# Kernel optimization log

Hardware: AMD Instinct MI355X
Metric: run time of the kernel (lower is better)

The kernel has to match this reference:

```python
import jax, jax.numpy as jnp
import numpy as np
from jax.scipy.special import logsumexp

DEN_SCALE = 1.0  # den_scale from LFMMILoss.__init__


def _log_marginal(em, seqlens, logA, log_start, log_final):
    """Forward (alpha) recursion of a WFSA in log space.
    em: [B,T,S] per-state emission log-likelihoods; logA: [S,S] or [B,S,S].
    Returns per-sequence log-marginal [B].
    """
    B, T, S = em.shape
    alpha0 = log_start + em[:, 0]  # [B,S]

    def step(alpha, xs):
        em_t, t = xs
        # [B,S,1] + [.,S,S] -> logsumexp over source state
        new = logsumexp(alpha[:, :, None] + logA, axis=1) + em_t
        alpha = jnp.where((t < seqlens)[:, None], new, alpha)
        return alpha, None

    em_t_first = jnp.swapaxes(em, 0, 1)  # [T,B,S]
    alpha, _ = jax.lax.scan(step, alpha0, (em_t_first[1:], jnp.arange(1, T)))
    return logsumexp(alpha + log_final, axis=1)  # [B]


def _fsm_logprob(x, seqlens, logA, log_start, log_final, pdf_ids):
    B, T, _ = x.shape
    if pdf_ids.ndim == 1:  # shared graph (denominator)
        em = x[:, :, pdf_ids]  # [B,T,S]
    else:  # per-utterance graphs (numerators), pdf_ids: [B,S]
        S = pdf_ids.shape[-1]
        idx = jnp.broadcast_to(pdf_ids[:, None, :], (B, T, S))
        em = jnp.take_along_axis(x, idx, axis=2)
    return _log_marginal(em, seqlens, logA, log_start, log_final)


def setup_inputs() -> dict:
    key = jax.random.key(0)
    ks = jax.random.split(key, 10)
    B, T, C = 16, 500, 2048
    S_num, S_den = 64, 512
    inp = jax.random.normal(ks[0], (B, T, C), jnp.float32)
    seqlengths = jax.random.randint(ks[1], (B,), T // 2, T + 1, jnp.int32)
    num_logA = jax.nn.log_softmax(jax.random.normal(ks[2], (B, S_num, S_num), jnp.float32), axis=-1)
    num_log_start = jax.nn.log_softmax(jax.random.normal(ks[3], (B, S_num), jnp.float32), axis=-1)
    num_log_final = jax.nn.log_softmax(jax.random.normal(ks[4], (B, S_num), jnp.float32), axis=-1)
    num_pdf_ids = jax.random.randint(ks[5], (B, S_num), 0, C, jnp.int32)
    den_logA = jax.nn.log_softmax(jax.random.normal(ks[6], (S_den, S_den), jnp.float32), axis=-1)
    den_log_start = jax.nn.log_softmax(jax.random.normal(ks[7], (S_den,), jnp.float32), axis=-1)
    den_log_final = jax.nn.log_softmax(jax.random.normal(ks[8], (S_den,), jnp.float32), axis=-1)
    den_pdf_ids = jax.random.randint(ks[9], (S_den,), 0, C, jnp.int32)
    return {
        "input": inp, "seqlengths": seqlengths,
        "num_logA": num_logA, "num_log_start": num_log_start,
        "num_log_final": num_log_final, "num_pdf_ids": num_pdf_ids,
        "den_logA": den_logA, "den_log_start": den_log_start,
        "den_log_final": den_log_final, "den_pdf_ids": den_pdf_ids,
    }


def reference(input, seqlengths, num_logA, num_log_start, num_log_final,
              num_pdf_ids, den_logA, den_log_start, den_log_final, den_pdf_ids):
    x = jnp.clip(input, -30.0, 30.0)
    num_llh = _fsm_logprob(x, seqlengths, num_logA, num_log_start, num_log_final, num_pdf_ids).sum()
    den_llh = _fsm_logprob(x, seqlengths, den_logA, den_log_start, den_log_final, den_pdf_ids).sum()
    return -(num_llh - DEN_SCALE * den_llh)
```

## Files before the change

kernel.cpp:

```cpp
#include <hip/hip_runtime.h>
#include <math.h>

#define BB 16
#define TT 500
#define CC 2048
#define SN 64
#define SD 512
#define NGRP 16
#define NCB 8
#define NDEN 128
#define NTHR 512
#define SHIFTC 30.0f

#define WSF_DACC   32768
#define WSF_DSCALE 32784
#define WSF_NACC   32800
#define WSF_NSCALE 32816

#define AL(p) __hip_atomic_load((p), __ATOMIC_RELAXED, __HIP_MEMORY_SCOPE_AGENT)
#define AS(p, v) __hip_atomic_store((p), (v), __ATOMIC_RELAXED, __HIP_MEMORY_SCOPE_AGENT)

__device__ __forceinline__ float wave_max(float v) {
  #pragma unroll
  for (int off = 32; off > 0; off >>= 1) v = fmaxf(v, __shfl_xor(v, off, 64));
  return v;
}
__device__ __forceinline__ float wave_sum(float v) {
  #pragma unroll
  for (int off = 32; off > 0; off >>= 1) v += __shfl_xor(v, off, 64);
  return v;
}
__device__ __forceinline__ unsigned long long pk(unsigned tag, float v) {
  return ((unsigned long long)tag << 32) | (unsigned long long)__float_as_uint(v);
}
__device__ __forceinline__ float clamp30(float v) {
  return fminf(fmaxf(v, -30.f), 30.f);
}

__global__ __launch_bounds__(NTHR, 1) void fsm_fwd(
    const float* __restrict__ x, const int* __restrict__ seqlens,
    const float* __restrict__ nA, const float* __restrict__ nls,
    const float* __restrict__ nlf, const int* __restrict__ npdf,
    const float* __restrict__ dA, const float* __restrict__ dls,
    const float* __restrict__ dlf, const int* __restrict__ dpdf,
    unsigned long long* __restrict__ p64, float* __restrict__ wsf)
{
  __shared__ float prt[2][8 * 64];
  __shared__ float pmx[2][8];
  const int tid = threadIdx.x;
  const int lane = tid & 63, wv = tid >> 6;

  if (blockIdx.x < NDEN) {
    const int g  = blockIdx.x & 15;
    const int cb = blockIdx.x >> 4;
    const int j0 = cb * 64;

    float Areg[64];
    {
      const float* Ap = dA + (wv * 64) * SD + j0 + lane;
      #pragma unroll
      for (int k = 0; k < 64; ++k)
        Areg[k] = __expf(Ap[k * SD]);
    }

    unsigned long long* gb0 = p64 + (size_t)g * SD;
    unsigned long long* gb1 = p64 + (size_t)(NGRP + g) * SD;

    int pdfj = 0, sl = 0; float lfj = 0.f, pcur = 0.f, scale = SHIFTC;
    if (wv == 0) {
      pdfj = dpdf[j0 + lane];
      lfj  = dlf[j0 + lane];
      sl   = seqlens[g];
      float xv = clamp30(x[g * (TT * CC) + pdfj]);
      pcur = __expf(dls[j0 + lane] + xv - SHIFTC);
      AS(gb0 + j0 + lane, pk(0u, pcur));
    }

    for (int t = 1; t < TT; ++t) {
      unsigned long long* gin  = (t & 1) ? gb0 : gb1;
      unsigned long long* gout = (t & 1) ? gb1 : gb0;
      float xv = 0.f;
      if (wv == 0)
        xv = clamp30(x[g * (TT * CC) + t * CC + pdfj]);

      const unsigned tg = (unsigned)(t - 1);
      unsigned long long* pa = gin + wv * 64 + lane;
      unsigned long long w;
      for (;;) {
        w = AL(pa);
        if ((unsigned)(w >> 32) == tg) break;
        __builtin_amdgcn_s_sleep(1);
      }
      float pv = __uint_as_float((unsigned)w);

      float cm = wave_max(pv);
      if (lane == 0) pmx[t & 1][wv] = cm;

      float q = 0.f;
      #pragma unroll
      for (int k = 0; k < 64; ++k) {
        float pk_ = __uint_as_float(__builtin_amdgcn_readlane(__float_as_uint(pv), k));
        q = fmaf(pk_, Areg[k], q);
      }
      prt[t & 1][wv * 64 + lane] = q;
      __syncthreads();

      if (wv == 0) {
        const float* pb = prt[t & 1];
        float qq = 0.f;
        #pragma unroll
        for (int w8 = 0; w8 < 8; ++w8) qq += pb[w8 * 64 + lane];
        float m = pmx[t & 1][0];
        #pragma unroll
        for (int w8 = 1; w8 < 8; ++w8) m = fmaxf(m, pmx[t & 1][w8]);
        float lm = __logf(m);
        if (t < sl) {
          pcur = qq * __expf(xv - SHIFTC - lm);
          scale += SHIFTC + lm;
        }
        AS(gout + j0 + lane, pk((unsigned)t, pcur));
      }
    }
    if (wv == 0) {
      float part = wave_sum(pcur * __expf(lfj));
      if (lane == 0) {
        atomicAdd(wsf + WSF_DACC + g, part);
        if (cb == 0) wsf[WSF_DSCALE + g] = scale;
      }
    }
  } else {
    const int b = blockIdx.x - NDEN;
    if (wv != 0) return;

    float Areg[64];
    {
      const float* Ap = nA + b * SN * SN + lane;
      #pragma unroll
      for (int i = 0; i < 64; ++i)
        Areg[i] = __expf(Ap[i * SN]);
    }
    const int   pdfj = npdf[b * SN + lane];
    const float lfj  = nlf[b * SN + lane];
    const int   sl   = seqlens[b];
    float xv = clamp30(x[b * (TT * CC) + pdfj]);
    float pcur = __expf(nls[b * SN + lane] + xv - SHIFTC);
    float scale = SHIFTC;

    for (int t = 1; t < TT; ++t) {
      xv = clamp30(x[b * (TT * CC) + t * CC + pdfj]);
      float pold = pcur;
      float q = 0.f;
      #pragma unroll
      for (int i = 0; i < 64; ++i) {
        float pi = __uint_as_float(__builtin_amdgcn_readlane(__float_as_uint(pold), i));
        q = fmaf(pi, Areg[i], q);
      }
      float lm = __logf(wave_max(pold));
      if (t < sl) {
        pcur = q * __expf(xv - SHIFTC - lm);
        scale += SHIFTC + lm;
      }
    }
    float part = wave_sum(pcur * __expf(lfj));
    if (lane == 0) {
      wsf[WSF_NACC + b]   = part;
      wsf[WSF_NSCALE + b] = scale;
    }
  }
}

__global__ void fsm_final(const float* __restrict__ wsf, float* __restrict__ out) {
  const int tid = threadIdx.x;
  float v = 0.f;
  if (tid < 16)
    v = -(wsf[WSF_NSCALE + tid] + __logf(wsf[WSF_NACC + tid]));
  else if (tid < 32)
    v = (wsf[WSF_DSCALE + tid - 16] + __logf(wsf[WSF_DACC + tid - 16]));
  v = wave_sum(v);
  if (tid == 0) out[0] = v;
}

extern "C" void kernel_launch(void* const* d_in, const int* in_sizes, int n_in,
                              void* d_out, int out_size, void* d_ws, size_t ws_size,
                              hipStream_t stream) {
  const float* x    = (const float*)d_in[0];
  const int*   sql  = (const int*)d_in[1];
  const float* nA   = (const float*)d_in[2];
  const float* nls  = (const float*)d_in[3];
  const float* nlf  = (const float*)d_in[4];
  const int*   npdf = (const int*)d_in[5];
  const float* dA   = (const float*)d_in[6];
  const float* dls  = (const float*)d_in[7];
  const float* dlf  = (const float*)d_in[8];
  const int*   dpdf = (const int*)d_in[9];
  float* out = (float*)d_out;
  unsigned long long* p64 = (unsigned long long*)d_ws;
  float* wsf = (float*)d_ws;
  (void)in_sizes; (void)n_in; (void)out_size; (void)ws_size;

  hipMemsetAsync((char*)d_ws + 131072, 0, 256, stream);
  fsm_fwd<<<NDEN + BB, NTHR, 0, stream>>>(x, sql, nA, nls, nlf, npdf,
                                          dA, dls, dlf, dpdf, p64, wsf);
  fsm_final<<<1, 64, 0, stream>>>(wsf, out);
}
```

Baseline: 892.4 us.

## Replace gather-then-reduce alpha exchange with distributed partial-sum reduce-scatter across blocks

The denominator recursion no longer funnels each step through wave 0. Previously wave 0 published 64 alpha values, every wave polled the full vector from global memory, and partials were reduced in LDS. Now every wave keeps its own 64-state slice of alpha and publishes per-(block, wave) partial products tagged with the step. Each wave then polls and sums the eight partials for its slice, so the serial wave-0 stage and one LDS reduction round are removed from the critical per-step path. In exchange there is more global polling traffic (eight tagged loads per lane), a larger workspace, and redundant alpha state in all eight blocks per group. Because each group's final sum is written by a single block, the atomic accumulation and the workspace memset are dropped.

```diff
diff --git a/kernel.cpp b/kernel.cpp
--- a/kernel.cpp
+++ b/kernel.cpp
@@ -6,16 +6,15 @@
 #define CC 2048
 #define SN 64
 #define SD 512
-#define NGRP 16
-#define NCB 8
 #define NDEN 128
 #define NTHR 512
 #define SHIFTC 30.0f
 
-#define WSF_DACC   32768
-#define WSF_DSCALE 32784
-#define WSF_NACC   32800
-#define WSF_NSCALE 32816
+#define PBUFO ((size_t)(16 * 8 * 8 * 64))
+#define WSF_DACC   262144
+#define WSF_DSCALE 262160
+#define WSF_NACC   262176
+#define WSF_NSCALE 262192
 
 #define AL(p) __hip_atomic_load((p), __ATOMIC_RELAXED, __HIP_MEMORY_SCOPE_AGENT)
 #define AS(p, v) __hip_atomic_store((p), (v), __ATOMIC_RELAXED, __HIP_MEMORY_SCOPE_AGENT)
@@ -45,8 +44,8 @@
     const float* __restrict__ dlf, const int* __restrict__ dpdf,
     unsigned long long* __restrict__ p64, float* __restrict__ wsf)
 {
-  __shared__ float prt[2][8 * 64];
   __shared__ float pmx[2][8];
+  __shared__ float red[8];
   const int tid = threadIdx.x;
   const int lane = tid & 63, wv = tid >> 6;
 
@@ -54,79 +53,92 @@
     const int g  = blockIdx.x & 15;
     const int cb = blockIdx.x >> 4;
     const int j0 = cb * 64;
+    const int i0 = wv * 64;
+    const int si = i0 + lane;
 
     float Areg[64];
     {
-      const float* Ap = dA + (wv * 64) * SD + j0 + lane;
+      const float* Ap = dA + (size_t)i0 * SD + j0 + lane;
       #pragma unroll
       for (int k = 0; k < 64; ++k)
-        Areg[k] = __expf(Ap[k * SD]);
-    }
-
-    unsigned long long* gb0 = p64 + (size_t)g * SD;
-    unsigned long long* gb1 = p64 + (size_t)(NGRP + g) * SD;
-
-    int pdfj = 0, sl = 0; float lfj = 0.f, pcur = 0.f, scale = SHIFTC;
-    if (wv == 0) {
-      pdfj = dpdf[j0 + lane];
-      lfj  = dlf[j0 + lane];
-      sl   = seqlens[g];
-      float xv = clamp30(x[g * (TT * CC) + pdfj]);
-      pcur = __expf(dls[j0 + lane] + xv - SHIFTC);
-      AS(gb0 + j0 + lane, pk(0u, pcur));
-    }
+        Areg[k] = __expf(Ap[(size_t)k * SD]);
+    }
+
+    const int   pdfj = dpdf[si];
+    const float lfj  = dlf[si];
+    const int   sl   = seqlens[g];
+    const float* xb  = x + (size_t)g * TT * CC;
+
+    float pwin  = __expf(dls[si] + clamp30(xb[pdfj]) - SHIFTC);
+    float scale = SHIFTC;
+    {
+      float wm = wave_max(pwin);
+      if (lane == 0) pmx[0][wv] = wm;
+    }
+    __syncthreads();
+    float lm;
+    {
+      float m = pmx[0][0];
+      #pragma unroll
+      for (int r = 1; r < 8; ++r) m = fmaxf(m, pmx[0][r]);
+      lm = __logf(m);
+    }
+
+    unsigned long long* myrow = p64 + (((size_t)g * 8 + cb) * 8 + wv) * 64;
+    unsigned long long* prows = p64 + (((size_t)g * 8 + wv) * 8) * 64;
 
     for (int t = 1; t < TT; ++t) {
-      unsigned long long* gin  = (t & 1) ? gb0 : gb1;
-      unsigned long long* gout = (t & 1) ? gb1 : gb0;
-      float xv = 0.f;
-      if (wv == 0)
-        xv = clamp30(x[g * (TT * CC) + t * CC + pdfj]);
-
-      const unsigned tg = (unsigned)(t - 1);
-      unsigned long long* pa = gin + wv * 64 + lane;
-      unsigned long long w;
-      for (;;) {
-        w = AL(pa);
-        if ((unsigned)(w >> 32) == tg) break;
-        __builtin_amdgcn_s_sleep(1);
-      }
-      float pv = __uint_as_float((unsigned)w);
-
-      float cm = wave_max(pv);
-      if (lane == 0) pmx[t & 1][wv] = cm;
+      const size_t bo = (t & 1) ? PBUFO : 0;
+      float xq = clamp30(xb[(size_t)t * CC + pdfj]);
 
       float q = 0.f;
       #pragma unroll
       for (int k = 0; k < 64; ++k) {
-        float pk_ = __uint_as_float(__builtin_amdgcn_readlane(__float_as_uint(pv), k));
-        q = fmaf(pk_, Areg[k], q);
-      }
-      prt[t & 1][wv * 64 + lane] = q;
+        float pv = __uint_as_float(__builtin_amdgcn_readlane(__float_as_uint(pwin), k));
+        q = fmaf(pv, Areg[k], q);
+      }
+      AS(myrow + bo + lane, pk((unsigned)t, q));
+
+      unsigned long long wr[8];
+      const unsigned tg = (unsigned)t;
+      unsigned long long* pr = prows + bo + lane;
+      unsigned miss = 0xFFu;
+      do {
+        #pragma unroll
+        for (int r = 0; r < 8; ++r)
+          if (miss & (1u << r)) wr[r] = AL(pr + r * 64);
+        #pragma unroll
+        for (int r = 0; r < 8; ++r)
+          if ((miss & (1u << r)) && (unsigned)(wr[r] >> 32) == tg) miss &= ~(1u << r);
+      } while (miss);
+
+      float s = 0.f;
+      #pragma unroll
+      for (int r = 0; r < 8; ++r) s += __uint_as_float((unsigned)wr[r]);
+      if (t < sl) {
+        pwin = s * __expf(xq - SHIFTC - lm);
+        scale += SHIFTC + lm;
+      }
+      float wm = wave_max(pwin);
+      if (lane == 0) pmx[t & 1][wv] = wm;
       __syncthreads();
-
-      if (wv == 0) {
-        const float* pb = prt[t & 1];
-        float qq = 0.f;
-        #pragma unroll
-        for (int w8 = 0; w8 < 8; ++w8) qq += pb[w8 * 64 + lane];
+      {
         float m = pmx[t & 1][0];
         #pragma unroll
-        for (int w8 = 1; w8 < 8; ++w8) m = fmaxf(m, pmx[t & 1][w8]);
-        float lm = __logf(m);
-        if (t < sl) {
-          pcur = qq * __expf(xv - SHIFTC - lm);
-          scale += SHIFTC + lm;
-        }
-        AS(gout + j0 + lane, pk((unsigned)t, pcur));
-      }
-    }
-    if (wv == 0) {
-      float part = wave_sum(pcur * __expf(lfj));
-      if (lane == 0) {
-        atomicAdd(wsf + WSF_DACC + g, part);
-        if (cb == 0) wsf[WSF_DSCALE + g] = scale;
-      }
+        for (int r = 1; r < 8; ++r) m = fmaxf(m, pmx[t & 1][r]);
+        lm = __logf(m);
+      }
+    }
+
+    float part = wave_sum(pwin * __expf(lfj));
+    if (lane == 0) red[wv] = part;
+    __syncthreads();
+    if (cb == 0 && tid == 0) {
+      float sum = 0.f;
+      #pragma unroll
+      for (int r = 0; r < 8; ++r) sum += red[r];
+      wsf[WSF_DACC + g]   = sum;
+      wsf[WSF_DSCALE + g] = scale;
     }
   } else {
     const int b = blockIdx.x - NDEN;
@@ -142,12 +154,12 @@
     const int   pdfj = npdf[b * SN + lane];
     const float lfj  = nlf[b * SN + lane];
     const int   sl   = seqlens[b];
-    float xv = clamp30(x[b * (TT * CC) + pdfj]);
+    float xv = clamp30(x[(size_t)b * TT * CC + pdfj]);
     float pcur = __expf(nls[b * SN + lane] + xv - SHIFTC);
     float scale = SHIFTC;
 
     for (int t = 1; t < TT; ++t) {
-      xv = clamp30(x[b * (TT * CC) + t * CC + pdfj]);
+      xv = clamp30(x[(size_t)b * TT * CC + t * CC + pdfj]);
       float pold = pcur;
       float q = 0.f;
       #pragma unroll
@@ -198,7 +210,6 @@
   float* wsf = (float*)d_ws;
   (void)in_sizes; (void)n_in; (void)out_size; (void)ws_size;
 
-  hipMemsetAsync((char*)d_ws + 131072, 0, 256, stream);
   fsm_fwd<<<NDEN + BB, NTHR, 0, stream>>>(x, sql, nA, nls, nlf, npdf,
                                           dA, dls, dlf, dpdf, p64, wsf);
   fsm_final<<<1, 64, 0, stream>>>(wsf, out);
```

Measured after the change: 1.349 ms. 51.1% more time.

## Replace per-step block barrier with tagged LDS flags and a dedicated reducer wave

Applied to the files above, without the earlier changes.

Each denominator block now has a ninth wave that only reduces and publishes results. The eight compute waves write tagged partial sums and maxima into shared memory and no longer wait on a __syncthreads each time step. The reducer wave polls those tags, combines the partials, applies the emission, and publishes alpha to global memory. This is meant to remove the per-step block barrier and let compute waves start on the next step's global poll while the reducer works. In exchange it adds spin-polling on LDS and a larger block of 576 threads.

```diff
diff --git a/kernel.cpp b/kernel.cpp
--- a/kernel.cpp
+++ b/kernel.cpp
@@ -6,10 +6,8 @@
 #define CC 2048
 #define SN 64
 #define SD 512
-#define NGRP 16
-#define NCB 8
 #define NDEN 128
-#define NTHR 512
+#define NTHR 576
 #define SHIFTC 30.0f
 
 #define WSF_DACC   32768
@@ -19,6 +17,8 @@
 
 #define AL(p) __hip_atomic_load((p), __ATOMIC_RELAXED, __HIP_MEMORY_SCOPE_AGENT)
 #define AS(p, v) __hip_atomic_store((p), (v), __ATOMIC_RELAXED, __HIP_MEMORY_SCOPE_AGENT)
+#define LL(p) __hip_atomic_load((p), __ATOMIC_RELAXED, __HIP_MEMORY_SCOPE_WORKGROUP)
+#define LS(p, v) __hip_atomic_store((p), (v), __ATOMIC_RELAXED, __HIP_MEMORY_SCOPE_WORKGROUP)
 
 __device__ __forceinline__ float wave_max(float v) {
   #pragma unroll
@@ -45,8 +45,8 @@
     const float* __restrict__ dlf, const int* __restrict__ dpdf,
     unsigned long long* __restrict__ p64, float* __restrict__ wsf)
 {
-  __shared__ float prt[2][8 * 64];
-  __shared__ float pmx[2][8];
+  __shared__ unsigned long long part[2][8][64];
+  __shared__ unsigned long long pmax[2][8];
   const int tid = threadIdx.x;
   const int lane = tid & 63, wv = tid >> 6;
 
@@ -54,77 +54,89 @@
     const int g  = blockIdx.x & 15;
     const int cb = blockIdx.x >> 4;
     const int j0 = cb * 64;
-
-    float Areg[64];
-    {
-      const float* Ap = dA + (wv * 64) * SD + j0 + lane;
-      #pragma unroll
-      for (int k = 0; k < 64; ++k)
-        Areg[k] = __expf(Ap[k * SD]);
-    }
-
     unsigned long long* gb0 = p64 + (size_t)g * SD;
-    unsigned long long* gb1 = p64 + (size_t)(NGRP + g) * SD;
-
-    int pdfj = 0, sl = 0; float lfj = 0.f, pcur = 0.f, scale = SHIFTC;
-    if (wv == 0) {
-      pdfj = dpdf[j0 + lane];
-      lfj  = dlf[j0 + lane];
-      sl   = seqlens[g];
-      float xv = clamp30(x[g * (TT * CC) + pdfj]);
-      pcur = __expf(dls[j0 + lane] + xv - SHIFTC);
-      AS(gb0 + j0 + lane, pk(0u, pcur));
-    }
-
-    for (int t = 1; t < TT; ++t) {
-      unsigned long long* gin  = (t & 1) ? gb0 : gb1;
-      unsigned long long* gout = (t & 1) ? gb1 : gb0;
-      float xv = 0.f;
-      if (wv == 0)
-        xv = clamp30(x[g * (TT * CC) + t * CC + pdfj]);
-
-      const unsigned tg = (unsigned)(t - 1);
-      unsigned long long* pa = gin + wv * 64 + lane;
-      unsigned long long w;
-      for (;;) {
-        w = AL(pa);
-        if ((unsigned)(w >> 32) == tg) break;
-        __builtin_amdgcn_s_sleep(1);
-      }
-      float pv = __uint_as_float((unsigned)w);
-
-      float cm = wave_max(pv);
-      if (lane == 0) pmx[t & 1][wv] = cm;
-
-      float q = 0.f;
-      #pragma unroll
-      for (int k = 0; k < 64; ++k) {
-        float pk_ = __uint_as_float(__builtin_amdgcn_readlane(__float_as_uint(pv), k));
-        q = fmaf(pk_, Areg[k], q);
-      }
-      prt[t & 1][wv * 64 + lane] = q;
-      __syncthreads();
-
-      if (wv == 0) {
-        const float* pb = prt[t & 1];
-        float qq = 0.f;
-        #pragma unroll
-        for (int w8 = 0; w8 < 8; ++w8) qq += pb[w8 * 64 + lane];
-        float m = pmx[t & 1][0];
-        #pragma unroll
-        for (int w8 = 1; w8 < 8; ++w8) m = fmaxf(m, pmx[t & 1][w8]);
+    unsigned long long* gb1 = p64 + (size_t)(16 + g) * SD;
+
+    for (int i2 = tid; i2 < 2 * 8 * 64; i2 += NTHR)
+      ((unsigned long long*)part)[i2] = 0xFFFFFFFF00000000ull;
+    if (tid < 16) ((unsigned long long*)pmax)[tid] = 0xFFFFFFFF00000000ull;
+    __syncthreads();
+
+    if (wv < 8) {
+      float Areg[64];
+      {
+        const float* Ap = dA + (size_t)(wv * 64) * SD + j0 + lane;
+        #pragma unroll
+        for (int k = 0; k < 64; ++k)
+          Areg[k] = __expf(Ap[(size_t)k * SD]);
+      }
+      for (int t = 1; t < TT; ++t) {
+        unsigned long long* gin = (t & 1) ? gb0 : gb1;
+        const unsigned tg = (unsigned)(t - 1);
+        unsigned long long* pa = gin + wv * 64 + lane;
+        unsigned long long w;
+        for (;;) {
+          w = AL(pa);
+          if ((unsigned)(w >> 32) == tg) break;
+          __builtin_amdgcn_s_sleep(1);
+        }
+        float pwin = __uint_as_float((unsigned)w);
+        float cm = wave_max(pwin);
+        float q = 0.f;
+        #pragma unroll
+        for (int k = 0; k < 64; ++k) {
+          float pv = __uint_as_float(__builtin_amdgcn_readlane(__float_as_uint(pwin), k));
+          q = fmaf(pv, Areg[k], q);
+        }
+        LS(&part[t & 1][wv][lane], pk((unsigned)t, q));
+        if (lane == 0) LS(&pmax[t & 1][wv], pk((unsigned)t, cm));
+      }
+    } else {
+      const int   si   = j0 + lane;
+      const int   pdfj = dpdf[si];
+      const float lfj  = dlf[si];
+      const int   sl   = seqlens[g];
+      const float* xb  = x + (size_t)g * TT * CC;
+      float pcur  = __expf(dls[si] + clamp30(xb[pdfj]) - SHIFTC);
+      float scale = SHIFTC;
+      AS(gb0 + si, pk(0u, pcur));
+
+      for (int t = 1; t < TT; ++t) {
+        float xq = clamp30(xb[(size_t)t * CC + pdfj]);
+        const unsigned tg = (unsigned)t;
+        unsigned long long wr[8], wm[8];
+        unsigned miss = 0xFFu;
+        do {
+          #pragma unroll
+          for (int r = 0; r < 8; ++r)
+            if (miss & (1u << r)) {
+              wr[r] = LL(&part[t & 1][r][lane]);
+              wm[r] = LL(&pmax[t & 1][r]);
+            }
+          #pragma unroll
+          for (int r = 0; r < 8; ++r)
+            if ((miss & (1u << r)) &&
+                (unsigned)(wr[r] >> 32) == tg && (unsigned)(wm[r] >> 32) == tg)
+              miss &= ~(1u << r);
+        } while (miss);
+
+        float s = 0.f;
+        #pragma unroll
+        for (int r = 0; r < 8; ++r) s += __uint_as_float((unsigned)wr[r]);
+        float m = __uint_as_float((unsigned)wm[0]);
+        #pragma unroll
+        for (int r = 1; r < 8; ++r) m = fmaxf(m, __uint_as_float((unsigned)wm[r]));
         float lm = __logf(m);
         if (t < sl) {
-          pcur = qq * __expf(xv - SHIFTC - lm);
+          pcur = s * __expf(xq - SHIFTC - lm);
           scale += SHIFTC + lm;
         }
-        AS(gout + j0 + lane, pk((unsigned)t, pcur));
-      }
-    }
-    if (wv == 0) {
-      float part = wave_sum(pcur * __expf(lfj));
+        unsigned long long* gout = (t & 1) ? gb1 : gb0;
+        AS(gout + si, pk((unsigned)t, pcur));
+      }
+      float prt_ = wave_sum(pcur * __expf(lfj));
       if (lane == 0) {
-        atomicAdd(wsf + WSF_DACC + g, part);
+        atomicAdd(wsf + WSF_DACC + g, prt_);
         if (cb == 0) wsf[WSF_DSCALE + g] = scale;
       }
     }
@@ -142,12 +154,12 @@
     const int   pdfj = npdf[b * SN + lane];
     const float lfj  = nlf[b * SN + lane];
     const int   sl   = seqlens[b];
-    float xv = clamp30(x[b * (TT * CC) + pdfj]);
+    float xv = clamp30(x[(size_t)b * TT * CC + pdfj]);
     float pcur = __expf(nls[b * SN + lane] + xv - SHIFTC);
     float scale = SHIFTC;
 
     for (int t = 1; t < TT; ++t) {
-      xv = clamp30(x[b * (TT * CC) + t * CC + pdfj]);
+      xv = clamp30(x[(size_t)b * TT * CC + t * CC + pdfj]);
       float pold = pcur;
       float q = 0.f;
       #pragma unroll
@@ -161,9 +173,9 @@
         scale += SHIFTC + lm;
       }
     }
-    float part = wave_sum(pcur * __expf(lfj));
+    float part_ = wave_sum(pcur * __expf(lfj));
     if (lane == 0) {
-      wsf[WSF_NACC + b]   = part;
+      wsf[WSF_NACC + b]   = part_;
       wsf[WSF_NSCALE + b] = scale;
     }
   }
```

Result: slower. 990.6 us (+11.0%).
